# Optimization experiments

Measured on AMD Instinct MI355X. Metric: run time of the kernel, lower is better.

The kernel has to match this reference:

```python
import jax, jax.numpy as jnp
import numpy as np

N_NODES = 100000
N_EDGES = 1600000
HID = 256
HEADS = 4
HEAD_DIM = HID // HEADS
EPS = 1e-5


def _layernorm(x, g, b):
    mu = jnp.mean(x, axis=-1, keepdims=True)
    var = jnp.mean(jnp.square(x - mu), axis=-1, keepdims=True)
    return (x - mu) * jax.lax.rsqrt(var + EPS) * g + b


def setup_inputs() -> dict:
    key = jax.random.key(0)
    ks = jax.random.split(key, 16)
    s = 0.05  # small init, mimics xavier gain=0.1
    inp = {
        'h': jax.random.normal(ks[0], (N_NODES, HID), jnp.float32),
        'src': jax.random.randint(ks[1], (N_EDGES,), 0, N_NODES, jnp.int32),
        'dst': jax.random.randint(ks[2], (N_EDGES,), 0, N_NODES, jnp.int32),
        'Wq': jax.random.normal(ks[3], (HID, HID), jnp.float32) * s,
        'bq': jnp.zeros((HID,), jnp.float32),
        'Wk': jax.random.normal(ks[4], (HID, HID), jnp.float32) * s,
        'bk': jnp.zeros((HID,), jnp.float32),
        'Wv': jax.random.normal(ks[5], (HID, HID), jnp.float32) * s,
        'bv': jnp.zeros((HID,), jnp.float32),
        'Wo': jax.random.normal(ks[6], (HID, HID), jnp.float32) * s,
        'bo': jnp.zeros((HID,), jnp.float32),
        'W1': jax.random.normal(ks[7], (HID, 2 * HID), jnp.float32) * s,
        'b1': jnp.zeros((2 * HID,), jnp.float32),
        'W2': jax.random.normal(ks[8], (2 * HID, HID), jnp.float32) * s,
        'b2': jnp.zeros((HID,), jnp.float32),
        'g1': jnp.ones((HID,), jnp.float32),
        'be1': jnp.zeros((HID,), jnp.float32),
        'g2': jnp.ones((HID,), jnp.float32),
        'be2': jnp.zeros((HID,), jnp.float32),
    }
    return inp


def reference(h, src, dst, Wq, bq, Wk, bk, Wv, bv, Wo, bo, W1, b1, W2, b2, g1, be1, g2, be2):
    N = h.shape[0]
    scale = HEAD_DIM ** -0.5
    h_norm = _layernorm(h, g1, be1)
    Q = (h_norm @ Wq + bq).reshape(N, HEADS, HEAD_DIM)
    K = (h_norm @ Wk + bk).reshape(N, HEADS, HEAD_DIM)
    V = (h_norm @ Wv + bv).reshape(N, HEADS, HEAD_DIM)

    # per-edge attention logits: q from dst, k from src  -> [E, heads]
    logits = jnp.einsum('ehd,ehd->eh', Q[dst], K[src]) * scale

    # edge softmax grouped by destination node (dgl.ops.edge_softmax)
    seg_max = jax.ops.segment_max(logits, dst, num_segments=N)  # [N, heads]
    e = jnp.exp(logits - seg_max[dst])
    seg_sum = jax.ops.segment_sum(e, dst, num_segments=N)
    w = e / seg_sum[dst]  # [E, heads]

    # message = V[src] * attn ; aggregate by sum over incoming edges
    msg = V[src] * w[:, :, None]  # [E, heads, head_dim]
    h_new = jax.ops.segment_sum(msg, dst, num_segments=N).reshape(N, HID)

    h_attn = h_new @ Wo + bo
    h = h + h_attn  # dropout is identity in eval
    h2 = _layernorm(h, g2, be2)
    ffn = jax.nn.relu(h2 @ W1 + b1) @ W2 + b2
    return h + ffn
```

## Files before the change

### kernel.cpp

```cpp
#include <hip/hip_runtime.h>
#include <hip/hip_bf16.h>

#define NN 100000
#define NE 1600000

typedef __attribute__((ext_vector_type(8))) short bf16x8;
typedef __attribute__((ext_vector_type(4))) float f32x4;
typedef __attribute__((ext_vector_type(2))) float f32x2;
typedef __attribute__((ext_vector_type(2))) unsigned int u32x2;
typedef __attribute__((ext_vector_type(4))) unsigned int u32x4;

__device__ __forceinline__ float bf2f(unsigned short u) {
    union { unsigned int i; float f; } c; c.i = ((unsigned int)u) << 16; return c.f;
}
__device__ __forceinline__ unsigned short f2bf(float f) {
    union { float f; unsigned int i; } c; c.f = f;
    unsigned int lsb = (c.i >> 16) & 1u;
    c.i += 0x7FFFu + lsb;
    return (unsigned short)(c.i >> 16);
}
__device__ __forceinline__ u32x4 pack8bf(f32x4 a, f32x4 b) {
    u32x4 p;
    p.x = f2bf(a[0]) | ((unsigned int)f2bf(a[1]) << 16);
    p.y = f2bf(a[2]) | ((unsigned int)f2bf(a[3]) << 16);
    p.z = f2bf(b[0]) | ((unsigned int)f2bf(b[1]) << 16);
    p.w = f2bf(b[2]) | ((unsigned int)f2bf(b[3]) << 16);
    return p;
}
__device__ __forceinline__ unsigned int pack4fp8(f32x4 v) {
    unsigned int w = __builtin_amdgcn_cvt_pk_fp8_f32(v[0], v[1], 0, false);
    return __builtin_amdgcn_cvt_pk_fp8_f32(v[2], v[3], w, true);
}
__device__ __forceinline__ void gload_lds16(const void* g, void* l) {
    __builtin_amdgcn_global_load_lds(
        (const __attribute__((address_space(1))) void*)g,
        (__attribute__((address_space(3))) void*)l, 16, 0, 0);
}

__global__ __launch_bounds__(256) void ln_k(
    const float* __restrict__ x, const float* __restrict__ g,
    const float* __restrict__ b, unsigned short* __restrict__ y, int nrows)
{
    int w = threadIdx.x >> 6, lane = threadIdx.x & 63;
    int row = blockIdx.x * 4 + w;
    if (row >= nrows) return;
    const float4 xv = *(const float4*)(x + (size_t)row * 256 + lane * 4);
    float s  = xv.x + xv.y + xv.z + xv.w;
    float sq = xv.x*xv.x + xv.y*xv.y + xv.z*xv.z + xv.w*xv.w;
    #pragma unroll
    for (int m = 1; m < 64; m <<= 1) {
        s  += __shfl_xor(s,  m);
        sq += __shfl_xor(sq, m);
    }
    float mu  = s * (1.0f / 256.0f);
    float var = sq * (1.0f / 256.0f) - mu * mu;
    float r = rsqrtf(var + 1e-5f);
    float4 gv = *(const float4*)(g + lane * 4);
    float4 bv = *(const float4*)(b + lane * 4);
    ushort4 o;
    o.x = f2bf((xv.x - mu) * r * gv.x + bv.x);
    o.y = f2bf((xv.y - mu) * r * gv.y + bv.y);
    o.z = f2bf((xv.z - mu) * r * gv.z + bv.z);
    o.w = f2bf((xv.w - mu) * r * gv.w + bv.w);
    *(ushort4*)(y + (size_t)row * 256 + lane * 4) = o;
}

__global__ __launch_bounds__(256) void wcv_all_k(
    const float* __restrict__ Wq, const float* __restrict__ Wk, const float* __restrict__ Wv,
    const float* __restrict__ Wo, const float* __restrict__ W1, const float* __restrict__ W2,
    unsigned short* __restrict__ Wqkvt, unsigned short* __restrict__ Wot,
    unsigned short* __restrict__ W1t, unsigned short* __restrict__ W2t,
    const float* __restrict__ bq, const float* __restrict__ bk, const float* __restrict__ bv,
    float* __restrict__ bqkv)
{
    int id = blockIdx.x;
    int t = threadIdx.x;
    if (id == 512) {
        bqkv[t] = bq[t]; bqkv[256 + t] = bk[t]; bqkv[512 + t] = bv[t];
        return;
    }
    const float* W; unsigned short* Wt; int K, N, kx, ny;
    if (id < 192) {
        int grp = id >> 6, l = id & 63;
        W = (grp == 0) ? Wq : ((grp == 1) ? Wk : Wv);
        Wt = Wqkvt + grp * 256 * 256;
        K = 256; N = 256; kx = l & 7; ny = l >> 3;
    } else if (id < 256) {
        int l = id - 192; W = Wo; Wt = Wot; K = 256; N = 256; kx = l & 7; ny = l >> 3;
    } else if (id < 384) {
        int l = id - 256; W = W1; Wt = W1t; K = 256; N = 512; kx = l & 7; ny = l >> 3;
    } else {
        int l = id - 384; W = W2; Wt = W2t; K = 512; N = 256; kx = l & 15; ny = l >> 4;
    }
    __shared__ unsigned short tl[32][33];
    int bk2 = kx * 32, bn = ny * 32;
    int lx = t & 31, ly = t >> 5;
    #pragma unroll
    for (int r = 0; r < 32; r += 8)
        tl[ly + r][lx] = f2bf(W[(size_t)(bk2 + ly + r) * N + bn + lx]);
    __syncthreads();
    #pragma unroll
    for (int r = 0; r < 32; r += 8)
        Wt[(size_t)(bn + ly + r) * K + bk2 + lx] = tl[lx][ly + r];
}

template<int NBX, int OMODE, bool RELU, bool RES>
__global__ __launch_bounds__(512) void mgemm_k(
    const unsigned short* __restrict__ A, const unsigned short* __restrict__ Wt,
    const float* __restrict__ bias, void* __restrict__ outv, void* __restrict__ out2,
    const void* __restrict__ res, const float* __restrict__ g, const float* __restrict__ be,
    int M, int N, int K)
{
    __shared__ __align__(16) char lds[73728];
    const int t = threadIdx.x;
    const int lane = t & 63;
    const int wid = t >> 6;
    const int wm = wid >> 2, wn = wid & 3;

    int bmi, bni;
    if (NBX > 0) {
        const int nwg = gridDim.x;
        const int q = nwg >> 3, r = nwg & 7;
        const int xcd = blockIdx.x & 7, idx = blockIdx.x >> 3;
        const int wgid = (xcd < r) ? (xcd * (q + 1) + idx)
                                   : (r * (q + 1) + (xcd - r) * q + idx);
        bmi = wgid / NBX; bni = wgid - bmi * NBX;
    } else {
        bmi = blockIdx.y; bni = blockIdx.x;
    }
    const int bm = bmi * 128, bn = bni * 256;

    f32x4 acc[4][4] = {};

    const int ra_s = t >> 2;
    const int sa_s = (t & 3) ^ (ra_s & 3);
    const size_t arow = (size_t)min(bm + ra_s, M - 1) * K + sa_s * 8;
    const int rb0 = t >> 2;
    const int sb0 = (t & 3) ^ (rb0 & 3);
    const int rb1 = (512 + t) >> 2;
    const int sb1 = (t & 3) ^ (rb1 & 3);
    const size_t brow0 = (size_t)(bn + rb0) * K + sb0 * 8;
    const size_t brow1 = (size_t)(bn + rb1) * K + sb1 * 8;

    const int fr = lane & 15, fs = lane >> 4;
    const int rslot = fs ^ (fr & 3);

    const int KS = K >> 5;

#define STAGE(b, k0) { \
        unsigned short* Ab = (unsigned short*)(lds + (b) * 8192); \
        unsigned short* Bb = (unsigned short*)(lds + 24576 + (b) * 16384); \
        const int kk_ = (k0) << 5; \
        gload_lds16(A + arow + kk_, Ab + t * 8); \
        gload_lds16(Wt + brow0 + kk_, Bb + t * 8); \
        gload_lds16(Wt + brow1 + kk_, Bb + (512 + t) * 8); }

    STAGE(0, 0)
    STAGE(1, 1)
    int cur = 0;
    for (int ks = 0; ks < KS; ++ks) {
        if (ks + 1 < KS) asm volatile("s_waitcnt vmcnt(3)" ::: "memory");
        else             asm volatile("s_waitcnt vmcnt(0)" ::: "memory");
        __builtin_amdgcn_s_barrier();
        if (ks + 2 < KS) {
            int nb = cur + 2; if (nb >= 3) nb -= 3;
            STAGE(nb, ks + 2)
        }
        const unsigned short* As = (const unsigned short*)(lds + cur * 8192);
        const unsigned short* Bs = (const unsigned short*)(lds + 24576 + cur * 16384);
        bf16x8 af[4], bf[4];
        #pragma unroll
        for (int fm = 0; fm < 4; ++fm)
            af[fm] = *(const bf16x8*)&As[(wm * 64 + fm * 16 + fr) * 32 + rslot * 8];
        #pragma unroll
        for (int fn = 0; fn < 4; ++fn)
            bf[fn] = *(const bf16x8*)&Bs[(wn * 64 + fn * 16 + fr) * 32 + rslot * 8];
        #pragma unroll
        for (int fm = 0; fm < 4; ++fm)
            #pragma unroll
            for (int fn = 0; fn < 4; ++fn)
                acc[fm][fn] = __builtin_amdgcn_mfma_f32_16x16x32_bf16(
                    af[fm], bf[fn], acc[fm][fn], 0, 0, 0);
        if (++cur == 3) cur = 0;
    }
#undef STAGE
    __syncthreads();

    float* wl = (float*)(lds + wid * 4352);
    float* stats = (float*)(lds + 34816);
    const int rr = lane >> 2;
    const int c4 = (lane & 3) * 16;
    const int qg = lane >> 4;

    #pragma unroll
    for (int fm = 0; fm < 4; ++fm) {
        #pragma unroll
        for (int fn = 0; fn < 4; ++fn)
            #pragma unroll
            for (int i = 0; i < 4; ++i)
                wl[(qg * 4 + i) * 68 + fn * 16 + fr] = acc[fm][fn][i];
        f32x4 v0 = *(const f32x4*)&wl[rr * 68 + c4 + 0];
        f32x4 v1 = *(const f32x4*)&wl[rr * 68 + c4 + 4];
        f32x4 v2 = *(const f32x4*)&wl[rr * 68 + c4 + 8];
        f32x4 v3 = *(const f32x4*)&wl[rr * 68 + c4 + 12];
        const int rowg = bm + wm * 64 + fm * 16 + rr;
        const int colg = bn + wn * 64 + c4;
        if (rowg < M) {
            v0 += *(const f32x4*)&bias[colg + 0];
            v1 += *(const f32x4*)&bias[colg + 4];
            v2 += *(const f32x4*)&bias[colg + 8];
            v3 += *(const f32x4*)&bias[colg + 12];
            if (RES) {
                const float* rp = (const float*)res + (size_t)rowg * N + colg;
                v0 += *(const f32x4*)(rp + 0);
                v1 += *(const f32x4*)(rp + 4);
                v2 += *(const f32x4*)(rp + 8);
                v3 += *(const f32x4*)(rp + 12);
            }
            if (RELU) {
                #pragma unroll
                for (int j = 0; j < 4; ++j) {
                    v0[j] = fmaxf(v0[j], 0.f); v1[j] = fmaxf(v1[j], 0.f);
                    v2[j] = fmaxf(v2[j], 0.f); v3[j] = fmaxf(v3[j], 0.f);
                }
            }
        } else {
            v0 = 0.f; v1 = 0.f; v2 = 0.f; v3 = 0.f;
        }

        if (OMODE == 3) {
            acc[fm][0] = v0; acc[fm][1] = v1; acc[fm][2] = v2; acc[fm][3] = v3;
        } else if (rowg < M) {
            if (colg < 256) {
                unsigned short* op = (unsigned short*)outv + (size_t)rowg * 256 + colg;
                *(u32x4*)(op + 0) = pack8bf(v0, v1);
                *(u32x4*)(op + 8) = pack8bf(v2, v3);
            } else {
                u32x4 p8;
                p8.x = pack4fp8(v0); p8.y = pack4fp8(v1);
                p8.z = pack4fp8(v2); p8.w = pack4fp8(v3);
                *(u32x4*)((unsigned char*)out2 + (size_t)rowg * 512 + (colg - 256)) = p8;
            }
        }
    }

    if (OMODE == 3) {
        #pragma unroll
        for (int fm = 0; fm < 4; ++fm) {
            float s = 0.f, q = 0.f;
            #pragma unroll
            for (int j = 0; j < 4; ++j)
                #pragma unroll
                for (int c = 0; c < 4; ++c) {
                    float x = acc[fm][j][c];
                    s += x; q += x * x;
                }
            s += __shfl_xor(s, 1); q += __shfl_xor(q, 1);
            s += __shfl_xor(s, 2); q += __shfl_xor(q, 2);
            if ((lane & 3) == 0) {
                int rowl = wm * 64 + fm * 16 + rr;
                stats[rowl * 8 + wn * 2 + 0] = s;
                stats[rowl * 8 + wn * 2 + 1] = q;
            }
        }
        __syncthreads();
        #pragma unroll
        for (int fm = 0; fm < 4; ++fm) {
            const int rowl = wm * 64 + fm * 16 + rr;
            const int rowg = bm + rowl;
            float s = stats[rowl * 8 + 0] + stats[rowl * 8 + 2] + stats[rowl * 8 + 4] + stats[rowl * 8 + 6];
            float q = stats[rowl * 8 + 1] + stats[rowl * 8 + 3] + stats[rowl * 8 + 5] + stats[rowl * 8 + 7];
            float mu = s * (1.0f / 256.0f);
            float var = q * (1.0f / 256.0f) - mu * mu;
            float rstd = rsqrtf(var + 1e-5f);
            const int colg = bn + wn * 64 + c4;
            if (rowg < M) {
                unsigned short* mp = (unsigned short*)out2 + (size_t)rowg * 256 + colg;
                *(u32x4*)(mp + 0) = pack8bf(acc[fm][0], acc[fm][1]);
                *(u32x4*)(mp + 8) = pack8bf(acc[fm][2], acc[fm][3]);
                f32x4 nv[4];
                #pragma unroll
                for (int j = 0; j < 4; ++j) {
                    f32x4 gv = *(const f32x4*)&g[colg + j * 4];
                    f32x4 bv = *(const f32x4*)&be[colg + j * 4];
                    #pragma unroll
                    for (int c = 0; c < 4; ++c)
                        nv[j][c] = (acc[fm][j][c] - mu) * rstd * gv[c] + bv[c];
                }
                unsigned short* op = (unsigned short*)outv + (size_t)rowg * 256 + colg;
                *(u32x4*)(op + 0) = pack8bf(nv[0], nv[1]);
                *(u32x4*)(op + 8) = pack8bf(nv[2], nv[3]);
            }
        }
    }
}

__global__ __launch_bounds__(512) void mffn_k(
    const unsigned short* __restrict__ A,
    const unsigned short* __restrict__ W1t,
    const unsigned short* __restrict__ W2t,
    const float* __restrict__ b1, const float* __restrict__ b2,
    const unsigned short* __restrict__ hmid,
    float* __restrict__ out, int M)
{
    __shared__ __align__(16) char lds[163840];
    char* Alds = lds;
    char* Blds = lds + 65536;
    char* Flds = lds + 98304;

    const int t = threadIdx.x;
    const int lane = t & 63;
    const int wid = t >> 6;
    const int wm = wid >> 2, wn = wid & 3;
    const int bm = blockIdx.y * 128;
    const int fr = lane & 15, fs = lane >> 4;
    const int rslot = fs ^ (fr & 3);

    const int ra = t >> 2;
    const int sa = (t & 3) ^ (ra & 3);
    const size_t abase = (size_t)min(bm + ra, M - 1) * 256 + sa * 8;
    #pragma unroll
    for (int kc = 0; kc < 8; ++kc)
        gload_lds16(A + abase + kc * 32, Alds + kc * 8192 + t * 16);

    const int rb0 = t >> 2;
    const int sb0 = (t & 3) ^ (rb0 & 3);
    const int rb1 = (512 + t) >> 2;
    const int sb1 = (t & 3) ^ (rb1 & 3);

    f32x4 acc2[4][4] = {};

    const int rr = lane >> 2;
    const int qg = lane >> 4;
    const int c4 = (lane & 3) * 16;

    for (int nh = 0; nh < 2; ++nh) {
        f32x4 acc1[4][4] = {};
        {
            const unsigned short* B1 = W1t + (size_t)(nh * 256) * 256;
            gload_lds16(B1 + (size_t)rb0 * 256 + sb0 * 8, Blds + t * 16);
            gload_lds16(B1 + (size_t)rb1 * 256 + sb1 * 8, Blds + 8192 + t * 16);
            int cur = 0;
            for (int ks = 0; ks < 8; ++ks) {
                __syncthreads();
                if (ks < 7) {
                    char* bb = Blds + (cur ^ 1) * 16384;
                    gload_lds16(B1 + (size_t)rb0 * 256 + sb0 * 8 + (ks + 1) * 32, bb + t * 16);
                    gload_lds16(B1 + (size_t)rb1 * 256 + sb1 * 8 + (ks + 1) * 32, bb + 8192 + t * 16);
                }
                const unsigned short* As = (const unsigned short*)(Alds + ks * 8192);
                const unsigned short* Bs = (const unsigned short*)(Blds + cur * 16384);
                bf16x8 af[4], bf[4];
                #pragma unroll
                for (int fm = 0; fm < 4; ++fm)
                    af[fm] = *(const bf16x8*)&As[(wm * 64 + fm * 16 + fr) * 32 + rslot * 8];
                #pragma unroll
                for (int fn = 0; fn < 4; ++fn)
                    bf[fn] = *(const bf16x8*)&Bs[(wn * 64 + fn * 16 + fr) * 32 + rslot * 8];
                #pragma unroll
                for (int fm = 0; fm < 4; ++fm)
                    #pragma unroll
                    for (int fn = 0; fn < 4; ++fn)
                        acc1[fm][fn] = __builtin_amdgcn_mfma_f32_16x16x32_bf16(
                            af[fm], bf[fn], acc1[fm][fn], 0, 0, 0);
                cur ^= 1;
            }
        }

        u32x4 pk[4][2];
        {
            float* wl = (float*)(Flds + wid * 4352);
            #pragma unroll
            for (int fm = 0; fm < 4; ++fm) {
                #pragma unroll
                for (int fn = 0; fn < 4; ++fn)
                    #pragma unroll
                    for (int i = 0; i < 4; ++i)
                        wl[(qg * 4 + i) * 68 + fn * 16 + fr] = acc1[fm][fn][i];
                f32x4 v0 = *(const f32x4*)&wl[rr * 68 + c4 + 0];
                f32x4 v1 = *(const f32x4*)&wl[rr * 68 + c4 + 4];
                f32x4 v2 = *(const f32x4*)&wl[rr * 68 + c4 + 8];
                f32x4 v3 = *(const f32x4*)&wl[rr * 68 + c4 + 12];
                const int colg = wn * 64 + c4;
                v0 += *(const f32x4*)&b1[nh * 256 + colg + 0];
                v1 += *(const f32x4*)&b1[nh * 256 + colg + 4];
                v2 += *(const f32x4*)&b1[nh * 256 + colg + 8];
                v3 += *(const f32x4*)&b1[nh * 256 + colg + 12];
                #pragma unroll
                for (int j = 0; j < 4; ++j) {
                    v0[j] = fmaxf(v0[j], 0.f); v1[j] = fmaxf(v1[j], 0.f);
                    v2[j] = fmaxf(v2[j], 0.f); v3[j] = fmaxf(v3[j], 0.f);
                }
                pk[fm][0] = pack8bf(v0, v1);
                pk[fm][1] = pack8bf(v2, v3);
            }
        }
        __syncthreads();

        {
            const int cg = wn * 64 + c4;
            const int kc = cg >> 5;
            const int o1 = (cg >> 3) & 3;
            #pragma unroll
            for (int fm = 0; fm < 4; ++fm) {
                const int row = wm * 64 + fm * 16 + rr;
                char* base = Flds + kc * 8192 + row * 64;
                *(u32x4*)(base + ((o1 ^ (row & 3)) * 16))       = pk[fm][0];
                *(u32x4*)(base + (((o1 + 1) ^ (row & 3)) * 16)) = pk[fm][1];
            }
        }
        __syncthreads();

        {
            const unsigned short* B2 = W2t + nh * 256;
            gload_lds16(B2 + (size_t)rb0 * 512 + sb0 * 8, Blds + t * 16);
            gload_lds16(B2 + (size_t)rb1 * 512 + sb1 * 8, Blds + 8192 + t * 16);
            int cur = 0;
            for (int ks = 0; ks < 8; ++ks) {
                __syncthreads();
                if (ks < 7) {
                    char* bb = Blds + (cur ^ 1) * 16384;
                    gload_lds16(B2 + (size_t)rb0 * 512 + sb0 * 8 + (ks + 1) * 32, bb + t * 16);
                    gload_lds16(B2 + (size_t)rb1 * 512 + sb1 * 8 + (ks + 1) * 32, bb + 8192 + t * 16);
                }
                const unsigned short* Fs = (const unsigned short*)(Flds + ks * 8192);
                const unsigned short* Bs = (const unsigned short*)(Blds + cur * 16384);
                bf16x8 af[4], bf[4];
                #pragma unroll
                for (int fm = 0; fm < 4; ++fm)
                    af[fm] = *(const bf16x8*)&Fs[(wm * 64 + fm * 16 + fr) * 32 + rslot * 8];
                #pragma unroll
                for (int fn = 0; fn < 4; ++fn)
                    bf[fn] = *(const bf16x8*)&Bs[(wn * 64 + fn * 16 + fr) * 32 + rslot * 8];
                #pragma unroll
                for (int fm = 0; fm < 4; ++fm)
                    #pragma unroll
                    for (int fn = 0; fn < 4; ++fn)
                        acc2[fm][fn] = __builtin_amdgcn_mfma_f32_16x16x32_bf16(
                            af[fm], bf[fn], acc2[fm][fn], 0, 0, 0);
                cur ^= 1;
            }
        }
        __syncthreads();
    }

    float* wl = (float*)(Alds + wid * 4352);
    #pragma unroll
    for (int fm = 0; fm < 4; ++fm) {
        #pragma unroll
        for (int fn = 0; fn < 4; ++fn)
            #pragma unroll
            for (int i = 0; i < 4; ++i)
                wl[(qg * 4 + i) * 68 + fn * 16 + fr] = acc2[fm][fn][i];
        f32x4 v0 = *(const f32x4*)&wl[rr * 68 + c4 + 0];
        f32x4 v1 = *(const f32x4*)&wl[rr * 68 + c4 + 4];
        f32x4 v2 = *(const f32x4*)&wl[rr * 68 + c4 + 8];
        f32x4 v3 = *(const f32x4*)&wl[rr * 68 + c4 + 12];
        const int rowg = bm + wm * 64 + fm * 16 + rr;
        const int colg = wn * 64 + c4;
        if (rowg < M) {
            v0 += *(const f32x4*)&b2[colg + 0];
            v1 += *(const f32x4*)&b2[colg + 4];
            v2 += *(const f32x4*)&b2[colg + 8];
            v3 += *(const f32x4*)&b2[colg + 12];
            const unsigned short* rp = hmid + (size_t)rowg * 256 + colg;
            u32x4 ra4 = *(const u32x4*)rp;
            u32x4 rb4 = *(const u32x4*)(rp + 8);
            v0[0] += bf2f(ra4.x & 0xffff); v0[1] += bf2f(ra4.x >> 16);
            v0[2] += bf2f(ra4.y & 0xffff); v0[3] += bf2f(ra4.y >> 16);
            v1[0] += bf2f(ra4.z & 0xffff); v1[1] += bf2f(ra4.z >> 16);
            v1[2] += bf2f(ra4.w & 0xffff); v1[3] += bf2f(ra4.w >> 16);
            v2[0] += bf2f(rb4.x & 0xffff); v2[1] += bf2f(rb4.x >> 16);
            v2[2] += bf2f(rb4.y & 0xffff); v2[3] += bf2f(rb4.y >> 16);
            v3[0] += bf2f(rb4.z & 0xffff); v3[1] += bf2f(rb4.z >> 16);
            v3[2] += bf2f(rb4.w & 0xffff); v3[3] += bf2f(rb4.w >> 16);
            float* op = out + (size_t)rowg * 256 + colg;
            *(f32x4*)(op + 0) = v0; *(f32x4*)(op + 4) = v1;
            *(f32x4*)(op + 8) = v2; *(f32x4*)(op + 12) = v3;
        }
    }
}

__global__ void degcnt_k(const int* __restrict__ dst, int* __restrict__ deg, int E)
{
    int e = blockIdx.x * blockDim.x + threadIdx.x;
    if (e < E) atomicAdd(deg + dst[e], 1);
}

__global__ __launch_bounds__(1024) void scanA_k(int* __restrict__ a, int* __restrict__ aux, int n)
{
    __shared__ int wsum[16];
    __shared__ int wpre[16];
    int t = threadIdx.x, lane = t & 63, w = t >> 6;
    int i = blockIdx.x * 1024 + t;
    int v = (i < n) ? a[i] : 0;
    int s = v;
    #pragma unroll
    for (int d = 1; d < 64; d <<= 1) {
        int u = __shfl_up(s, d);
        if (lane >= d) s += u;
    }
    if (lane == 63) wsum[w] = s;
    __syncthreads();
    if (t == 0) {
        int run = 0;
        #pragma unroll
        for (int j = 0; j < 16; ++j) { wpre[j] = run; run += wsum[j]; }
        aux[blockIdx.x] = run;
    }
    __syncthreads();
    if (i < n) a[i] = wpre[w] + s - v;
}

__global__ __launch_bounds__(128) void scanB_k(int* __restrict__ aux, int* __restrict__ tot, int nb)
{
    __shared__ int ws[2];
    int t = threadIdx.x, lane = t & 63, w = t >> 6;
    int v = (t < nb) ? aux[t] : 0;
    int s = v;
    #pragma unroll
    for (int d = 1; d < 64; d <<= 1) {
        int u = __shfl_up(s, d);
        if (lane >= d) s += u;
    }
    if (lane == 63) ws[w] = s;
    __syncthreads();
    int add = (w == 1) ? ws[0] : 0;
    if (t < nb) aux[t] = add + s - v;
    if (t == nb - 1) tot[0] = add + s;
}

__global__ __launch_bounds__(1024) void scanC_k(int* __restrict__ a, const int* __restrict__ aux, int n)
{
    int i = blockIdx.x * 1024 + threadIdx.x;
    if (i < n) a[i] += aux[blockIdx.x];
}

__global__ void scatter_k(
    const int* __restrict__ dst, const int* __restrict__ srcarr,
    const int* __restrict__ off, int* __restrict__ cursor,
    int* __restrict__ csr, int E)
{
    int e = blockIdx.x * blockDim.x + threadIdx.x;
    if (e >= E) return;
    int d = dst[e];
    int pos = off[d] + atomicAdd(cursor + d, 1);
    csr[pos] = srcarr[e];
}

__global__ __launch_bounds__(256) void attn_k(
    const int* __restrict__ csr, const int* __restrict__ off,
    const unsigned short* __restrict__ Q, const unsigned char* __restrict__ KV8,
    unsigned short* __restrict__ hnew)
{
    int w = threadIdx.x >> 6, lane = threadIdx.x & 63;
    int n = blockIdx.x * 4 + w;
    if (n >= NN) return;
    int e0 = off[n], e1 = off[n + 1];
    int hl = lane & 31, par = lane >> 5;

    const float qs = 0.125f * 1.4426950408889634f;
    f32x2 q01, q23, q45, q67;
    {
        u32x4 qa = __builtin_nontemporal_load((const u32x4*)(Q + (size_t)n * 256 + hl * 8));
        q01[0] = bf2f((unsigned short)(qa.x & 0xffff)) * qs;
        q01[1] = bf2f((unsigned short)(qa.x >> 16)) * qs;
        q23[0] = bf2f((unsigned short)(qa.y & 0xffff)) * qs;
        q23[1] = bf2f((unsigned short)(qa.y >> 16)) * qs;
        q45[0] = bf2f((unsigned short)(qa.z & 0xffff)) * qs;
        q45[1] = bf2f((unsigned short)(qa.z >> 16)) * qs;
        q67[0] = bf2f((unsigned short)(qa.w & 0xffff)) * qs;
        q67[1] = bf2f((unsigned short)(qa.w >> 16)) * qs;
    }
    f32x2 a01 = {0.f, 0.f}, a23 = {0.f, 0.f}, a45 = {0.f, 0.f}, a67 = {0.f, 0.f};
    float s = 0.f;
    const unsigned char* KVl = KV8 + hl * 8;

    int i = e0;
    for (; i + 7 < e1; i += 8) {
        int b[4];
        #pragma unroll
        for (int t2 = 0; t2 < 4; ++t2) b[t2] = csr[i + 2 * t2 + par] << 9;
        u32x2 kd[4], vd[4];
        #pragma unroll
        for (int t2 = 0; t2 < 4; ++t2) {
            kd[t2] = *(const u32x2*)(KVl + (unsigned)b[t2]);
            vd[t2] = *(const u32x2*)(KVl + (unsigned)b[t2] + 256);
        }
        #pragma unroll
        for (int t2 = 0; t2 < 4; ++t2) {
            f32x2 lv = q01 * __builtin_amdgcn_cvt_pk_f32_fp8(kd[t2].x, false);
            lv += q23 * __builtin_amdgcn_cvt_pk_f32_fp8(kd[t2].x, true);
            lv += q45 * __builtin_amdgcn_cvt_pk_f32_fp8(kd[t2].y, false);
            lv += q67 * __builtin_amdgcn_cvt_pk_f32_fp8(kd[t2].y, true);
            float l = lv[0] + lv[1];
            l += __shfl_xor(l, 1);
            l += __shfl_xor(l, 2);
            l += __shfl_xor(l, 4);
            float p = exp2f(l);
            s += p;
            f32x2 pp = {p, p};
            a01 += pp * __builtin_amdgcn_cvt_pk_f32_fp8(vd[t2].x, false);
            a23 += pp * __builtin_amdgcn_cvt_pk_f32_fp8(vd[t2].x, true);
            a45 += pp * __builtin_amdgcn_cvt_pk_f32_fp8(vd[t2].y, false);
            a67 += pp * __builtin_amdgcn_cvt_pk_f32_fp8(vd[t2].y, true);
        }
    }
    for (; i < e1; i += 2) {
        int eidx = i + par;
        int idx = (eidx < e1) ? eidx : (e1 - 1);
        int b = csr[idx] << 9;
        u32x2 kd = *(const u32x2*)(KVl + (unsigned)b);
        u32x2 vd = *(const u32x2*)(KVl + (unsigned)b + 256);
        f32x2 lv = q01 * __builtin_amdgcn_cvt_pk_f32_fp8(kd.x, false);
        lv += q23 * __builtin_amdgcn_cvt_pk_f32_fp8(kd.x, true);
        lv += q45 * __builtin_amdgcn_cvt_pk_f32_fp8(kd.y, false);
        lv += q67 * __builtin_amdgcn_cvt_pk_f32_fp8(kd.y, true);
        float l = lv[0] + lv[1];
        l += __shfl_xor(l, 1);
        l += __shfl_xor(l, 2);
        l += __shfl_xor(l, 4);
        float p = (eidx < e1) ? exp2f(l) : 0.f;
        s += p;
        f32x2 pp = {p, p};
        a01 += pp * __builtin_amdgcn_cvt_pk_f32_fp8(vd.x, false);
        a23 += pp * __builtin_amdgcn_cvt_pk_f32_fp8(vd.x, true);
        a45 += pp * __builtin_amdgcn_cvt_pk_f32_fp8(vd.y, false);
        a67 += pp * __builtin_amdgcn_cvt_pk_f32_fp8(vd.y, true);
    }

    a01[0] += __shfl_xor(a01[0], 32); a01[1] += __shfl_xor(a01[1], 32);
    a23[0] += __shfl_xor(a23[0], 32); a23[1] += __shfl_xor(a23[1], 32);
    a45[0] += __shfl_xor(a45[0], 32); a45[1] += __shfl_xor(a45[1], 32);
    a67[0] += __shfl_xor(a67[0], 32); a67[1] += __shfl_xor(a67[1], 32);
    s += __shfl_xor(s, 32);

    float inv = (e1 > e0) ? 1.0f / s : 0.f;
    if (par == 0) {
        u32x4 ov;
        ov.x = f2bf(a01[0] * inv) | ((unsigned int)f2bf(a01[1] * inv) << 16);
        ov.y = f2bf(a23[0] * inv) | ((unsigned int)f2bf(a23[1] * inv) << 16);
        ov.z = f2bf(a45[0] * inv) | ((unsigned int)f2bf(a45[1] * inv) << 16);
        ov.w = f2bf(a67[0] * inv) | ((unsigned int)f2bf(a67[1] * inv) << 16);
        __builtin_nontemporal_store(ov, (u32x4*)(hnew + (size_t)n * 256 + hl * 8));
    }
}

extern "C" void kernel_launch(void* const* d_in, const int* in_sizes, int n_in,
                              void* d_out, int out_size, void* d_ws, size_t ws_size,
                              hipStream_t stream)
{
    if (n_in < 19) return;
    const float* h   = (const float*)d_in[0];
    const int*   src = (const int*)d_in[1];
    const int*   dst = (const int*)d_in[2];
    const float* Wq  = (const float*)d_in[3];
    const float* bq  = (const float*)d_in[4];
    const float* Wk  = (const float*)d_in[5];
    const float* bk  = (const float*)d_in[6];
    const float* Wv  = (const float*)d_in[7];
    const float* bv  = (const float*)d_in[8];
    const float* Wo  = (const float*)d_in[9];
    const float* bo  = (const float*)d_in[10];
    const float* W1  = (const float*)d_in[11];
    const float* b1  = (const float*)d_in[12];
    const float* W2  = (const float*)d_in[13];
    const float* b2  = (const float*)d_in[14];
    const float* g1  = (const float*)d_in[15];
    const float* be1 = (const float*)d_in[16];
    const float* g2  = (const float*)d_in[17];
    const float* be2 = (const float*)d_in[18];
    float* out = (float*)d_out;

    char* w = (char*)d_ws;
    unsigned short* hnormb = (unsigned short*)(w + 0);
    unsigned short* Qb     = (unsigned short*)(w + 51200000);
    unsigned char*  KV8    = (unsigned char*)(w + 102400000);
    int*            degoff = (int*)(w + 153600000);
    int*            cursor = (int*)(w + 154000384);
    int*            csr    = (int*)(w + 154400768);
    unsigned short* Wqkvt  = (unsigned short*)(w + 204800000);
    unsigned short* Wot    = (unsigned short*)(w + 205193216);
    unsigned short* W1t    = (unsigned short*)(w + 205324288);
    unsigned short* W2t    = (unsigned short*)(w + 205586432);
    float*          bqkv   = (float*)(w + 205848576);
    int*            scanaux= (int*)(w + 205851648);
    unsigned short* hnewb  = hnormb;
    unsigned short* h2nb   = hnormb;
    unsigned short* hmidb  = Qb;

    hipMemsetAsync(degoff, 0, 400384, stream);
    hipMemsetAsync(cursor, 0, 400384, stream);

    const int M = NN;
    dim3 blk(256);
    dim3 blk512(512);
    const int MB = (M + 127) / 128;
    const int SCAN_BLKS = (NN + 1023) / 1024;

    wcv_all_k<<<dim3(513), blk, 0, stream>>>(Wq, Wk, Wv, Wo, W1, W2,
                                             Wqkvt, Wot, W1t, W2t, bq, bk, bv, bqkv);

    degcnt_k<<<dim3((NE + 255) / 256), blk, 0, stream>>>(dst, degoff, NE);
    scanA_k<<<dim3(SCAN_BLKS), dim3(1024), 0, stream>>>(degoff, scanaux, NN);
    scanB_k<<<dim3(1), dim3(128), 0, stream>>>(scanaux, degoff + NN, SCAN_BLKS);
    scanC_k<<<dim3(SCAN_BLKS), dim3(1024), 0, stream>>>(degoff, scanaux, NN);
    scatter_k<<<dim3((NE + 255) / 256), blk, 0, stream>>>(dst, src, degoff, cursor, csr, NE);

    ln_k<<<dim3((NN + 3) / 4), blk, 0, stream>>>(h, g1, be1, hnormb, NN);

    mgemm_k<3, 2, false, false><<<dim3(3 * MB), blk512, 0, stream>>>(
        hnormb, Wqkvt, bqkv, Qb, KV8, nullptr, nullptr, nullptr, M, 768, 256);

    attn_k<<<dim3((NN + 3) / 4), blk, 0, stream>>>(csr, degoff, Qb, KV8, hnewb);

    dim3 go(1, MB);
    mgemm_k<0, 3, false, true><<<go, blk512, 0, stream>>>(
        hnewb, Wot, bo, h2nb, hmidb, h, g2, be2, M, 256, 256);

    mffn_k<<<go, blk512, 0, stream>>>(h2nb, W1t, W2t, b1, b2, hmidb, out, M);
}
```

Measured before the change: 576.0 us.

## Halve FFN row tile to 64 and shrink LDS for higher occupancy

Cuts the fused FFN kernel's row tile from 128 to 64 rows, halving A/F LDS buffers and accumulator registers, and adds a launch-bounds occupancy hint so more blocks fit per CU. The B-operand double buffering is removed in favour of a single buffer with a load then sync then compute pattern, which frees more LDS. This aims to raise occupancy and give more blocks across the CUs. The cost is that each weight tile is reloaded for twice as many blocks, and without the prefetch global-load latency is no longer hidden inside a block.

```diff
diff --git a/kernel.cpp b/kernel.cpp
--- a/kernel.cpp
+++ b/kernel.cpp
@@ -295,7 +295,7 @@
     }
 }
 
-__global__ __launch_bounds__(512) void mffn_k(
+__global__ __launch_bounds__(512, 4) void mffn_k(
     const unsigned short* __restrict__ A,
     const unsigned short* __restrict__ W1t,
     const unsigned short* __restrict__ W2t,
@@ -303,75 +303,74 @@
     const unsigned short* __restrict__ hmid,
     float* __restrict__ out, int M)
 {
-    __shared__ __align__(16) char lds[163840];
+    __shared__ __align__(16) char lds[81920];
     char* Alds = lds;
-    char* Blds = lds + 65536;
-    char* Flds = lds + 98304;
+    char* Blds = lds + 32768;
+    char* Flds = lds + 49152;
 
     const int t = threadIdx.x;
     const int lane = t & 63;
     const int wid = t >> 6;
     const int wm = wid >> 2, wn = wid & 3;
-    const int bm = blockIdx.y * 128;
+    const int bm = blockIdx.y * 64;
     const int fr = lane & 15, fs = lane >> 4;
     const int rslot = fs ^ (fr & 3);
 
-    const int ra = t >> 2;
-    const int sa = (t & 3) ^ (ra & 3);
-    const size_t abase = (size_t)min(bm + ra, M - 1) * 256 + sa * 8;
-    #pragma unroll
-    for (int kc = 0; kc < 8; ++kc)
-        gload_lds16(A + abase + kc * 32, Alds + kc * 8192 + t * 16);
+    {
+        const int tt = t & 255, tc = t >> 8;
+        const int rowA = tt >> 2;
+        const int slotA = (tt & 3) ^ (rowA & 3);
+        const size_t abase = (size_t)min(bm + rowA, M - 1) * 256 + slotA * 8;
+        #pragma unroll
+        for (int kc0 = 0; kc0 < 8; kc0 += 2) {
+            int kc = kc0 + tc;
+            gload_lds16(A + abase + kc * 32, Alds + kc * 4096 + tt * 16);
+        }
+    }
 
     const int rb0 = t >> 2;
     const int sb0 = (t & 3) ^ (rb0 & 3);
     const int rb1 = (512 + t) >> 2;
     const int sb1 = (t & 3) ^ (rb1 & 3);
 
-    f32x4 acc2[4][4] = {};
-
+    f32x4 acc2[2][4] = {};
     const int rr = lane >> 2;
     const int qg = lane >> 4;
     const int c4 = (lane & 3) * 16;
 
     for (int nh = 0; nh < 2; ++nh) {
-        f32x4 acc1[4][4] = {};
+        f32x4 acc1[2][4] = {};
         {
             const unsigned short* B1 = W1t + (size_t)(nh * 256) * 256;
-            gload_lds16(B1 + (size_t)rb0 * 256 + sb0 * 8, Blds + t * 16);
-            gload_lds16(B1 + (size_t)rb1 * 256 + sb1 * 8, Blds + 8192 + t * 16);
-            int cur = 0;
             for (int ks = 0; ks < 8; ++ks) {
                 __syncthreads();
-                if (ks < 7) {
-                    char* bb = Blds + (cur ^ 1) * 16384;
-                    gload_lds16(B1 + (size_t)rb0 * 256 + sb0 * 8 + (ks + 1) * 32, bb + t * 16);
-                    gload_lds16(B1 + (size_t)rb1 * 256 + sb1 * 8 + (ks + 1) * 32, bb + 8192 + t * 16);
-                }
-                const unsigned short* As = (const unsigned short*)(Alds + ks * 8192);
-                const unsigned short* Bs = (const unsigned short*)(Blds + cur * 16384);
-                bf16x8 af[4], bf[4];
-                #pragma unroll
-                for (int fm = 0; fm < 4; ++fm)
-                    af[fm] = *(const bf16x8*)&As[(wm * 64 + fm * 16 + fr) * 32 + rslot * 8];
+                gload_lds16(B1 + (size_t)rb0 * 256 + sb0 * 8 + ks * 32, Blds + t * 16);
+                gload_lds16(B1 + (size_t)rb1 * 256 + sb1 * 8 + ks * 32, Blds + 8192 + t * 16);
+                __syncthreads();
+                const unsigned short* As = (const unsigned short*)(Alds + ks * 4096);
+                const unsigned short* Bs = (const unsigned short*)Blds;
+                bf16x8 af[2], bf[4];
+                #pragma unroll
+                for (int fm = 0; fm < 2; ++fm)
+                    af[fm] = *(const bf16x8*)&As[(wm * 32 + fm * 16 + fr) * 32 + rslot * 8];
                 #pragma unroll
                 for (int fn = 0; fn < 4; ++fn)
                     bf[fn] = *(const bf16x8*)&Bs[(wn * 64 + fn * 16 + fr) * 32 + rslot * 8];
                 #pragma unroll
-                for (int fm = 0; fm < 4; ++fm)
+                for (int fm = 0; fm < 2; ++fm)
                     #pragma unroll
                     for (int fn = 0; fn < 4; ++fn)
                         acc1[fm][fn] = __builtin_amdgcn_mfma_f32_16x16x32_bf16(
                             af[fm], bf[fn], acc1[fm][fn], 0, 0, 0);
-                cur ^= 1;
-            }
-        }
-
-        u32x4 pk[4][2];
+            }
+        }
+        __syncthreads();
+
+        u32x4 pk[2][2];
         {
-            float* wl = (float*)(Flds + wid * 4352);
+            float* wl = (float*)(lds + 32768 + wid * 4352);
             #pragma unroll
-            for (int fm = 0; fm < 4; ++fm) {
+            for (int fm = 0; fm < 2; ++fm) {
                 #pragma unroll
                 for (int fn = 0; fn < 4; ++fn)
                     #pragma unroll
@@ -402,9 +401,9 @@
             const int kc = cg >> 5;
             const int o1 = (cg >> 3) & 3;
             #pragma unroll
-            for (int fm = 0; fm < 4; ++fm) {
-                const int row = wm * 64 + fm * 16 + rr;
-                char* base = Flds + kc * 8192 + row * 64;
+            for (int fm = 0; fm < 2; ++fm) {
+                const int row = wm * 32 + fm * 16 + rr;
+                char* base = Flds + kc * 4096 + row * 64;
                 *(u32x4*)(base + ((o1 ^ (row & 3)) * 16))       = pk[fm][0];
                 *(u32x4*)(base + (((o1 + 1) ^ (row & 3)) * 16)) = pk[fm][1];
             }
@@ -413,32 +412,26 @@
 
         {
             const unsigned short* B2 = W2t + nh * 256;
-            gload_lds16(B2 + (size_t)rb0 * 512 + sb0 * 8, Blds + t * 16);
-            gload_lds16(B2 + (size_t)rb1 * 512 + sb1 * 8, Blds + 8192 + t * 16);
-            int cur = 0;
             for (int ks = 0; ks < 8; ++ks) {
                 __syncthreads();
-                if (ks < 7) {
-                    char* bb = Blds + (cur ^ 1) * 16384;
-                    gload_lds16(B2 + (size_t)rb0 * 512 + sb0 * 8 + (ks + 1) * 32, bb + t * 16);
-                    gload_lds16(B2 + (size_t)rb1 * 512 + sb1 * 8 + (ks + 1) * 32, bb + 8192 + t * 16);
-                }
-                const unsigned short* Fs = (const unsigned short*)(Flds + ks * 8192);
-                const unsigned short* Bs = (const unsigned short*)(Blds + cur * 16384);
-                bf16x8 af[4], bf[4];
-                #pragma unroll
-                for (int fm = 0; fm < 4; ++fm)
-                    af[fm] = *(const bf16x8*)&Fs[(wm * 64 + fm * 16 + fr) * 32 + rslot * 8];
+                gload_lds16(B2 + (size_t)rb0 * 512 + sb0 * 8 + ks * 32, Blds + t * 16);
+                gload_lds16(B2 + (size_t)rb1 * 512 + sb1 * 8 + ks * 32, Blds + 8192 + t * 16);
+                __syncthreads();
+                const unsigned short* Fs = (const unsigned short*)(Flds + ks * 4096);
+                const unsigned short* Bs = (const unsigned short*)Blds;
+                bf16x8 af[2], bf[4];
+                #pragma unroll
+                for (int fm = 0; fm < 2; ++fm)
+                    af[fm] = *(const bf16x8*)&Fs[(wm * 32 + fm * 16 + fr) * 32 + rslot * 8];
                 #pragma unroll
                 for (int fn = 0; fn < 4; ++fn)
                     bf[fn] = *(const bf16x8*)&Bs[(wn * 64 + fn * 16 + fr) * 32 + rslot * 8];
                 #pragma unroll
-                for (int fm = 0; fm < 4; ++fm)
+                for (int fm = 0; fm < 2; ++fm)
                     #pragma unroll
                     for (int fn = 0; fn < 4; ++fn)
                         acc2[fm][fn] = __builtin_amdgcn_mfma_f32_16x16x32_bf16(
                             af[fm], bf[fn], acc2[fm][fn], 0, 0, 0);
-                cur ^= 1;
             }
         }
         __syncthreads();
@@ -446,7 +439,7 @@
 
     float* wl = (float*)(Alds + wid * 4352);
     #pragma unroll
-    for (int fm = 0; fm < 4; ++fm) {
+    for (int fm = 0; fm < 2; ++fm) {
         #pragma unroll
         for (int fn = 0; fn < 4; ++fn)
             #pragma unroll
@@ -456,7 +449,7 @@
         f32x4 v1 = *(const f32x4*)&wl[rr * 68 + c4 + 4];
         f32x4 v2 = *(const f32x4*)&wl[rr * 68 + c4 + 8];
         f32x4 v3 = *(const f32x4*)&wl[rr * 68 + c4 + 12];
-        const int rowg = bm + wm * 64 + fm * 16 + rr;
+        const int rowg = bm + wm * 32 + fm * 16 + rr;
         const int colg = wn * 64 + c4;
         if (rowg < M) {
             v0 += *(const f32x4*)&b2[colg + 0];
@@ -696,6 +689,7 @@
     dim3 blk(256);
     dim3 blk512(512);
     const int MB = (M + 127) / 128;
+    const int MB64 = (M + 63) / 64;
     const int SCAN_BLKS = (NN + 1023) / 1024;
 
     wcv_all_k<<<dim3(513), blk, 0, stream>>>(Wq, Wk, Wv, Wo, W1, W2,
@@ -718,5 +712,5 @@
     mgemm_k<0, 3, false, true><<<go, blk512, 0, stream>>>(
         hnewb, Wot, bo, h2nb, hmidb, h, g2, be2, M, 256, 256);
 
-    mffn_k<<<go, blk512, 0, stream>>>(h2nb, W1t, W2t, b1, b2, hmidb, out, M);
-}
+    mffn_k<<<dim3(1, MB64), blk512, 0, stream>>>(h2nb, W1t, W2t, b1, b2, hmidb, out, M);
+}
```

New measurement: 583.1 us. Within noise of the previous version (+1.2%).
